# Kernel optimization log

Hardware: AMD Instinct MI355X
Metric: run time of the kernel (lower is better)

The kernel has to match this reference:

```python
import jax, jax.numpy as jnp
import numpy as np

N_NODES = 50000


def _glorot(key, fan_in, fan_out):
    lim = jnp.sqrt(6.0 / (fan_in + fan_out)).astype(jnp.float32)
    return jax.random.uniform(key, (fan_in, fan_out), jnp.float32, -lim, lim)


def gcn_layer(x, W, b, src, dst, deg_inv_sqrt):
    # PyG GCNConv: x' = D^{-1/2} (A + I) D^{-1/2} (x W) + b
    h = x @ W  # [N, F_out]
    norm = deg_inv_sqrt[src] * deg_inv_sqrt[dst]  # [E+N]
    msg = norm[:, None] * h[src]                  # gather + scale
    out = jax.ops.segment_sum(msg, dst, num_segments=x.shape[0])
    return out + b


def setup_inputs() -> dict:
    key = jax.random.key(0)
    ks = jax.random.split(key, 8)
    in_c, out_c = 128, 64
    hid = 2 * out_c
    x = jax.random.normal(ks[0], (N_NODES, in_c), jnp.float32)
    edge_index = jax.random.randint(ks[1], (2, 800000), 0, N_NODES, jnp.int64)
    return {
        "x": x,
        "edge_index": edge_index,
        "W1": _glorot(ks[2], in_c, hid), "b1": jnp.zeros((hid,), jnp.float32),
        "W2": _glorot(ks[3], hid, hid),  "b2": jnp.zeros((hid,), jnp.float32),
        "W3": _glorot(ks[4], hid, out_c), "b3": jnp.zeros((out_c,), jnp.float32),
    }


def reference(x, edge_index, W1, b1, W2, b2, W3, b3):
    n = x.shape[0]
    loops = jnp.arange(n, dtype=edge_index.dtype)
    src = jnp.concatenate([edge_index[0], loops])  # [E+N]
    dst = jnp.concatenate([edge_index[1], loops])
    deg = jax.ops.segment_sum(jnp.ones_like(dst, dtype=x.dtype), dst, num_segments=n)
    deg_inv_sqrt = jnp.where(deg > 0, jax.lax.rsqrt(deg), 0.0)

    h = jax.nn.relu(gcn_layer(x, W1, b1, src, dst, deg_inv_sqrt))
    h = jax.nn.relu(gcn_layer(h, W2, b2, src, dst, deg_inv_sqrt))
    return gcn_layer(h, W3, b3, src, dst, deg_inv_sqrt)
```

## Files before the change

kernel.cpp:

```cpp
#include <hip/hip_runtime.h>
#include <hip/hip_bf16.h>
#include <hip/hip_fp16.h>
#include <cstdint>
#include <cstddef>

typedef _Float16 half8_t __attribute__((ext_vector_type(8)));
typedef float f32x4 __attribute__((ext_vector_type(4)));
typedef unsigned short ushort8_v __attribute__((ext_vector_type(8)));


__global__ __launch_bounds__(256) void prep_kernel(int* __restrict__ cnt, int N4,
                                                   const float* __restrict__ W1, _Float16* __restrict__ wt1,
                                                   const float* __restrict__ W2, _Float16* __restrict__ wt2,
                                                   const float* __restrict__ W3, _Float16* __restrict__ wt3,
                                                   _Float16* __restrict__ gA, _Float16* __restrict__ gB,
                                                   _Float16* __restrict__ gC, int N) {
  int i = blockIdx.x * 256 + threadIdx.x;
  if (i < N4) {
    *(int4*)&cnt[i * 4] = make_int4(0, 0, 0, 0);
    return;
  }
  int j = i - N4;
  if (j < 16384) {
    int k = j >> 7, c = j & 127;
    wt1[c * 128 + k] = (_Float16)W1[j];
    return;
  }
  j -= 16384;
  if (j < 16384) {
    int k = j >> 7, c = j & 127;
    wt2[c * 128 + k] = (_Float16)W2[j];
    return;
  }
  j -= 16384;
  if (j < 8192) {
    int k = j >> 6, c = j & 63;
    wt3[c * 128 + k] = (_Float16)W3[j];
    return;
  }
  j -= 8192;
  if (j < 40) {
    half8_t z = {};
    if (j < 16)       *(half8_t*)&gA[(size_t)N * 128 + j * 8] = z;
    else if (j < 32)  *(half8_t*)&gB[(size_t)N * 128 + (j - 16) * 8] = z;
    else              *(half8_t*)&gC[(size_t)N * 64 + (j - 32) * 8] = z;
  }
}


__global__ __launch_bounds__(256) void countpos_fill_kernel(const int* __restrict__ dst,
                                                            int* __restrict__ cnt,
                                                            ushort* __restrict__ pos, int E,
                                                            int* __restrict__ ssInt, int ssInts,
                                                            int countBlocks, int fillPat) {
  if (blockIdx.x >= countBlocks) {
    int f = ((blockIdx.x - countBlocks) * 256 + threadIdx.x) * 4;
    if (f + 4 <= ssInts) *(int4*)&ssInt[f] = make_int4(fillPat, fillPat, fillPat, fillPat);
    else for (; f < ssInts; ++f) ssInt[f] = fillPat;
    return;
  }
  int e = (blockIdx.x * blockDim.x + threadIdx.x) * 2;
  if (e + 2 <= E) {
    int2 d = *(const int2*)&dst[e];
    int p0 = atomicAdd(&cnt[d.x], 1);
    int p1 = atomicAdd(&cnt[d.y], 1);
    ushort2 pk;
    pk.x = (ushort)p0; pk.y = (ushort)p1;
    *(ushort2*)&pos[e] = pk;
  } else {
    for (; e < E; ++e) pos[e] = (ushort)atomicAdd(&cnt[dst[e]], 1);
  }
}


__global__ __launch_bounds__(256) void block_sum_kernel(const int* __restrict__ cnt,
                                                        int* __restrict__ bsum, int N) {
  const int tid = threadIdx.x, lane = tid & 63, wid = tid >> 6;
  __shared__ int wt[4];
  int base = blockIdx.x * 2048 + tid * 8;
  int s = 0;
#pragma unroll
  for (int q = 0; q < 8; ++q) { int i = base + q; if (i < N) s += (cnt[i] + 7) & ~7; }
#pragma unroll
  for (int off = 32; off; off >>= 1) s += __shfl_down(s, off);
  if (lane == 0) wt[wid] = s;
  __syncthreads();
  if (tid == 0) bsum[blockIdx.x] = wt[0] + wt[1] + wt[2] + wt[3];
}

__global__ __launch_bounds__(256) void scan_bsum_kernel(const int* __restrict__ bsum,
                                                        int* __restrict__ boff,
                                                        int NB, int* __restrict__ rpN) {
  __shared__ int sh[256];
  const int tid = threadIdx.x;
  int v = (tid < NB) ? bsum[tid] : 0;
  sh[tid] = v;
  __syncthreads();
  for (int off = 1; off < 256; off <<= 1) {
    int t = (tid >= off) ? sh[tid - off] : 0;
    __syncthreads();
    sh[tid] += t;
    __syncthreads();
  }
  if (tid < NB) boff[tid] = sh[tid] - v;
  if (tid == 255) rpN[0] = sh[255];
}

__global__ __launch_bounds__(256) void scan_apply_kernel(const int* __restrict__ cnt,
                                                         const int* __restrict__ boff,
                                                         int* __restrict__ rp,
                                                         float* __restrict__ dis, int N) {
  const int tid = threadIdx.x, lane = tid & 63, wid = tid >> 6;
  __shared__ int wtot[4], wexc[4];
  int base = blockIdx.x * 2048 + tid * 8;
  int v[8]; int s = 0;
#pragma unroll
  for (int q = 0; q < 8; ++q) {
    int i = base + q; int x = (i < N) ? cnt[i] : 0;
    v[q] = x; s += (x + 7) & ~7;
  }
  int sc = s;
#pragma unroll
  for (int off = 1; off < 64; off <<= 1) { int t = __shfl_up(sc, off); if (lane >= off) sc += t; }
  if (lane == 63) wtot[wid] = sc;
  __syncthreads();
  if (tid == 0) { int r = 0; for (int wq = 0; wq < 4; ++wq) { wexc[wq] = r; r += wtot[wq]; } }
  __syncthreads();
  int thr = boff[blockIdx.x] + wexc[wid] + (sc - s);
#pragma unroll
  for (int q = 0; q < 8; ++q) {
    int i = base + q;
    if (i < N) { rp[i] = thr; dis[i] = rsqrtf((float)(v[q] + 1)); }
    thr += (v[q] + 7) & ~7;
  }
}


__global__ __launch_bounds__(256) void place_gemm1_kernel(const int* __restrict__ src,
                                                          const int* __restrict__ dst,
                                                          const ushort* __restrict__ pos,
                                                          const int* __restrict__ rp,
                                                          ushort* __restrict__ ss, int E,
                                                          const float* __restrict__ X,
                                                          const half8_t* __restrict__ Wt,
                                                          const float* __restrict__ dis,
                                                          _Float16* __restrict__ G, int N,
                                                          int gemmBlocks) {
  if (blockIdx.x >= gemmBlocks) {
    int e = ((blockIdx.x - gemmBlocks) * blockDim.x + threadIdx.x) * 4;
    if (e + 4 <= E) {
      int4 d = *(const int4*)&dst[e];
      ushort4 p = *(const ushort4*)&pos[e];
      int4 s = *(const int4*)&src[e];
      int r0 = rp[d.x], r1 = rp[d.y], r2 = rp[d.z], r3 = rp[d.w];
      ss[r0 + p.x] = (ushort)s.x;
      ss[r1 + p.y] = (ushort)s.y;
      ss[r2 + p.z] = (ushort)s.z;
      ss[r3 + p.w] = (ushort)s.w;
    } else {
      for (; e < E; ++e) ss[rp[dst[e]] + pos[e]] = (ushort)src[e];
    }
    return;
  }
  const int wave = threadIdx.x >> 6;
  const int lane = threadIdx.x & 63;
  const int wm = wave >> 1, wn = wave & 1;
  const int row0 = blockIdx.x * 128 + wm * 64;
  const int col0 = wn * 64;
  const int lr = lane & 15;
  const int lk = lane >> 4;
  f32x4 acc[4][4];
#pragma unroll
  for (int r = 0; r < 4; ++r)
#pragma unroll
    for (int c = 0; c < 4; ++c) acc[r][c] = (f32x4){0.f, 0.f, 0.f, 0.f};

#pragma unroll
  for (int ks = 0; ks < 4; ++ks) {
    half8_t a[4], b[4];
#pragma unroll
    for (int r = 0; r < 4; ++r) {
      int row = row0 + r * 16 + lr;
      half8_t av = {};
      if (row < N) {
        const float* xp = &X[(size_t)row * 128 + ks * 32 + lk * 8];
        float4 xa = *(const float4*)xp;
        float4 xb = *(const float4*)(xp + 4);
        av[0] = (_Float16)xa.x; av[1] = (_Float16)xa.y; av[2] = (_Float16)xa.z; av[3] = (_Float16)xa.w;
        av[4] = (_Float16)xb.x; av[5] = (_Float16)xb.y; av[6] = (_Float16)xb.z; av[7] = (_Float16)xb.w;
      }
      a[r] = av;
    }
#pragma unroll
    for (int c = 0; c < 4; ++c) {
      int col = col0 + c * 16 + lr;
      b[c] = Wt[(size_t)col * 16 + ks * 4 + lk];
    }
#pragma unroll
    for (int r = 0; r < 4; ++r)
#pragma unroll
      for (int c = 0; c < 4; ++c)
        acc[r][c] = __builtin_amdgcn_mfma_f32_16x16x32_f16(a[r], b[c], acc[r][c], 0, 0, 0);
  }

#pragma unroll
  for (int r = 0; r < 4; ++r) {
#pragma unroll
    for (int q = 0; q < 4; ++q) {
      int row = row0 + r * 16 + lk * 4 + q;
      if (row < N) {
        float dv = dis[row];
#pragma unroll
        for (int c = 0; c < 4; ++c)
          G[(size_t)row * 128 + col0 + c * 16 + lr] = (_Float16)(acc[r][c][q] * dv);
      }
    }
  }
}


template <int COUT>
__global__ __launch_bounds__(256) void fused_agg_gemm_kernel(const _Float16* __restrict__ G,
                                                             const int* __restrict__ rp,
                                                             const ushort* __restrict__ ss,
                                                             const float* __restrict__ dis,
                                                             const float* __restrict__ bias,
                                                             const half8_t* __restrict__ Wt,
                                                             _Float16* __restrict__ G2, int N) {
  __shared__ _Float16 sh[32][136];
  const int wave = threadIdx.x >> 6;
  const int lane = threadIdx.x & 63;
  const int grp = lane >> 4;
  const int sub = lane & 15;
  const int nb0 = blockIdx.x * 32;

#pragma unroll
  for (int it = 0; it < 2; ++it) {
    const int wl = it * 16 + wave * 4 + grp;
    const int w = nb0 + wl;
    if (w < N) {
      const int e0 = rp[w], e1 = rp[w + 1];
      float acc[8];
      half8_t sv = *(const half8_t*)&G[(size_t)w * 128 + sub * 8];
#pragma unroll
      for (int j = 0; j < 8; ++j) acc[j] = (float)sv[j];
      for (int e = e0; e < e1; e += 8) {
        ushort8_v iv = *(const ushort8_v*)&ss[e];
        half8_t v[8];
#pragma unroll
        for (int q = 0; q < 8; ++q) v[q] = *(const half8_t*)&G[(size_t)iv[q] * 128 + sub * 8];
#pragma unroll
        for (int j = 0; j < 8; ++j)
          acc[j] += (((float)v[0][j] + (float)v[1][j]) + ((float)v[2][j] + (float)v[3][j])) +
                    (((float)v[4][j] + (float)v[5][j]) + ((float)v[6][j] + (float)v[7][j]));
      }
      float d = dis[w];
      float4 b0 = *(const float4*)&bias[sub * 8];
      float4 b1 = *(const float4*)&bias[sub * 8 + 4];
      float bb[8] = {b0.x, b0.y, b0.z, b0.w, b1.x, b1.y, b1.z, b1.w};
      half8_t o;
#pragma unroll
      for (int j = 0; j < 8; ++j) {
        float v = fmaxf(d * acc[j] + bb[j], 0.f);
        o[j] = (_Float16)v;
      }
      *(half8_t*)&sh[wl][sub * 8] = o;
    }
  }
  __syncthreads();

  const int lr = lane & 15;
  const int lk = lane >> 4;
  constexpr int NC = COUT / 64;
  const int col0 = wave * (COUT / 4);
  f32x4 acc2[2][NC];
#pragma unroll
  for (int r = 0; r < 2; ++r)
#pragma unroll
    for (int c = 0; c < NC; ++c) acc2[r][c] = (f32x4){0.f, 0.f, 0.f, 0.f};

#pragma unroll
  for (int ks = 0; ks < 4; ++ks) {
    half8_t a[2], b[NC];
#pragma unroll
    for (int r = 0; r < 2; ++r)
      a[r] = *(const half8_t*)&sh[r * 16 + lr][ks * 32 + lk * 8];
#pragma unroll
    for (int c = 0; c < NC; ++c) {
      int col = col0 + c * 16 + lr;
      b[c] = Wt[(size_t)col * 16 + ks * 4 + lk];
    }
#pragma unroll
    for (int r = 0; r < 2; ++r)
#pragma unroll
      for (int c = 0; c < NC; ++c)
        acc2[r][c] = __builtin_amdgcn_mfma_f32_16x16x32_f16(a[r], b[c], acc2[r][c], 0, 0, 0);
  }

#pragma unroll
  for (int r = 0; r < 2; ++r) {
#pragma unroll
    for (int q = 0; q < 4; ++q) {
      int row = nb0 + r * 16 + lk * 4 + q;
      if (row < N) {
        float dv = dis[row];
#pragma unroll
        for (int c = 0; c < NC; ++c)
          G2[(size_t)row * COUT + col0 + c * 16 + lr] = (_Float16)(acc2[r][c][q] * dv);
      }
    }
  }
}


__global__ __launch_bounds__(256) void agg64_kernel(const _Float16* __restrict__ G,
                                                    const int* __restrict__ rp,
                                                    const ushort* __restrict__ ss,
                                                    const float* __restrict__ dis,
                                                    const float* __restrict__ bias,
                                                    float* __restrict__ OUT, int N) {
  const int wave = threadIdx.x >> 6;
  const int lane = threadIdx.x & 63;
  const int grp = lane >> 3;
  const int sub = lane & 7;
  const int w = blockIdx.x * 32 + wave * 8 + grp;
  if (w >= N) return;
  const int e0 = rp[w], e1 = rp[w + 1];
  float acc[8];
  half8_t sv = *(const half8_t*)&G[(size_t)w * 64 + sub * 8];
#pragma unroll
  for (int j = 0; j < 8; ++j) acc[j] = (float)sv[j];
  for (int e = e0; e < e1; e += 8) {
    ushort8_v iv = *(const ushort8_v*)&ss[e];
    half8_t v[8];
#pragma unroll
    for (int q = 0; q < 8; ++q) v[q] = *(const half8_t*)&G[(size_t)iv[q] * 64 + sub * 8];
#pragma unroll
    for (int j = 0; j < 8; ++j)
      acc[j] += (((float)v[0][j] + (float)v[1][j]) + ((float)v[2][j] + (float)v[3][j])) +
                (((float)v[4][j] + (float)v[5][j]) + ((float)v[6][j] + (float)v[7][j]));
  }
  float d = dis[w];
  float4 b0 = *(const float4*)&bias[sub * 8];
  float4 b1 = *(const float4*)&bias[sub * 8 + 4];
  float4 o0, o1;
  o0.x = d * acc[0] + b0.x; o0.y = d * acc[1] + b0.y;
  o0.z = d * acc[2] + b0.z; o0.w = d * acc[3] + b0.w;
  o1.x = d * acc[4] + b1.x; o1.y = d * acc[5] + b1.y;
  o1.z = d * acc[6] + b1.z; o1.w = d * acc[7] + b1.w;
  *(float4*)&OUT[(size_t)w * 64 + sub * 8] = o0;
  *(float4*)&OUT[(size_t)w * 64 + sub * 8 + 4] = o1;
}


extern "C" void kernel_launch(void* const* d_in, const int* in_sizes, int n_in,
                              void* d_out, int out_size, void* d_ws, size_t ws_size,
                              hipStream_t stream) {
  const float* x  = (const float*)d_in[0];
  const int*   ei = (const int*)d_in[1];
  const float* W1 = (const float*)d_in[2];
  const float* b1 = (const float*)d_in[3];
  const float* W2 = (const float*)d_in[4];
  const float* b2 = (const float*)d_in[5];
  const float* W3 = (const float*)d_in[6];
  const float* b3 = (const float*)d_in[7];

  const int inC = in_sizes[2] / in_sizes[3];
  const int N = in_sizes[0] / inC;
  const int E = in_sizes[1] / 2;

  const int SSPAD = ((E + 7 * N + 8) + 7) & ~7;

  auto align256 = [](size_t v) { return (v + 255) & ~(size_t)255; };
  char* p = (char*)d_ws;
  int* cnt = (int*)p;   p += align256((size_t)N * 4);
  int* rp  = (int*)p;   p += align256((size_t)(N + 1) * 4);
  ushort* ss = (ushort*)p;  p += align256((size_t)SSPAD * 2);
  ushort* pos = (ushort*)p; p += align256((size_t)E * 2);
  float* dis = (float*)p; p += align256((size_t)N * 4);
  _Float16* gA = (_Float16*)p; p += align256((size_t)(N + 1) * 128 * 2);
  _Float16* gB = (_Float16*)p; p += align256((size_t)(N + 1) * 128 * 2);
  _Float16* gC = (_Float16*)p; p += align256((size_t)(N + 1) * 64 * 2);
  _Float16* wt1 = (_Float16*)p; p += align256((size_t)128 * 128 * 2);
  _Float16* wt2 = (_Float16*)p; p += align256((size_t)128 * 128 * 2);
  _Float16* wt3 = (_Float16*)p; p += align256((size_t)64 * 128 * 2);
  int* bsum = (int*)p;  p += align256(1024 * 4);
  int* boff = (int*)p;  p += align256(1024 * 4);

  const int* srcv = ei;
  const int* dstv = ei + E;

  const int NB = (N + 2047) / 2048;
  const int eB2 = (E / 2 + 255) / 256;
  const int eB4 = (E / 4 + 255) / 256;
  const int N4 = (N + 3) / 4;
  const int prepTot = N4 + 16384 + 16384 + 8192 + 40;
  const int ssInts = SSPAD / 2;
  const int fillB = (ssInts / 4 + 255) / 256;
  const int fillPat = (int)(((unsigned)N) | (((unsigned)N) << 16));

  prep_kernel<<<(prepTot + 255) / 256, 256, 0, stream>>>(cnt, N4, W1, wt1, W2, wt2, W3, wt3,
                                                         gA, gB, gC, N);
  countpos_fill_kernel<<<eB2 + fillB, 256, 0, stream>>>(dstv, cnt, pos, E,
                                                        (int*)ss, ssInts, eB2, fillPat);
  block_sum_kernel<<<NB, 256, 0, stream>>>(cnt, bsum, N);
  scan_bsum_kernel<<<1, 256, 0, stream>>>(bsum, boff, NB, rp + N);
  scan_apply_kernel<<<NB, 256, 0, stream>>>(cnt, boff, rp, dis, N);

  const int g1B = (N + 127) / 128;
  const int fB  = (N + 31) / 32;
  const int a64B = (N + 31) / 32;

  place_gemm1_kernel<<<g1B + eB4, 256, 0, stream>>>(srcv, dstv, pos, rp, ss, E,
                                                    x, (const half8_t*)wt1, dis, gA, N, g1B);
  fused_agg_gemm_kernel<128><<<fB, 256, 0, stream>>>(gA, rp, ss, dis, b1, (const half8_t*)wt2, gB, N);
  fused_agg_gemm_kernel<64><<<fB, 256, 0, stream>>>(gB, rp, ss, dis, b2, (const half8_t*)wt3, gC, N);
  agg64_kernel<<<a64B, 256, 0, stream>>>(gC, rp, ss, dis, b3, (float*)d_out, N);
}
```

Measured before the change: 167.9 us.

## Split feature columns into passes and spread edges across lanes in aggregation

Both aggregation kernels now go over the feature dimension in 32-column passes (four for the 128-wide layer, two for the 64-wide output). Within each pass, lanes that used to cover distinct feature slices are split into edge-parallel groups, with partial sums combined through xor shuffles. The intent is to keep each pass's gather working set small so neighbor rows stay in cache, and to cut per-lane outstanding loads and register pressure. In exchange, the index array and row offsets are re-read on every pass, shuffle reductions are added, and only a quarter or half of the lanes do the epilogue.

```diff
diff --git a/kernel.cpp b/kernel.cpp
--- a/kernel.cpp
+++ b/kernel.cpp
@@ -232,39 +232,53 @@
   const int lane = threadIdx.x & 63;
   const int grp = lane >> 4;
   const int sub = lane & 15;
+  const int ep = sub >> 2;
+  const int fq = sub & 3;
   const int nb0 = blockIdx.x * 32;
 
 #pragma unroll
-  for (int it = 0; it < 2; ++it) {
-    const int wl = it * 16 + wave * 4 + grp;
-    const int w = nb0 + wl;
-    if (w < N) {
-      const int e0 = rp[w], e1 = rp[w + 1];
-      float acc[8];
-      half8_t sv = *(const half8_t*)&G[(size_t)w * 128 + sub * 8];
-#pragma unroll
-      for (int j = 0; j < 8; ++j) acc[j] = (float)sv[j];
-      for (int e = e0; e < e1; e += 8) {
-        ushort8_v iv = *(const ushort8_v*)&ss[e];
-        half8_t v[8];
-#pragma unroll
-        for (int q = 0; q < 8; ++q) v[q] = *(const half8_t*)&G[(size_t)iv[q] * 128 + sub * 8];
-#pragma unroll
-        for (int j = 0; j < 8; ++j)
-          acc[j] += (((float)v[0][j] + (float)v[1][j]) + ((float)v[2][j] + (float)v[3][j])) +
-                    (((float)v[4][j] + (float)v[5][j]) + ((float)v[6][j] + (float)v[7][j]));
+  for (int pass = 0; pass < 4; ++pass) {
+#pragma unroll
+    for (int it = 0; it < 2; ++it) {
+      const int wl = it * 16 + wave * 4 + grp;
+      const int w = nb0 + wl;
+      if (w < N) {
+        const int e0 = rp[w], e1 = rp[w + 1];
+        float acc[8];
+        if (ep == 0) {
+          half8_t sv = *(const half8_t*)&G[(size_t)w * 128 + pass * 32 + fq * 8];
+#pragma unroll
+          for (int j = 0; j < 8; ++j) acc[j] = (float)sv[j];
+        } else {
+#pragma unroll
+          for (int j = 0; j < 8; ++j) acc[j] = 0.f;
+        }
+        for (int e = e0; e < e1; e += 8) {
+          ushort8_v iv = *(const ushort8_v*)&ss[e];
+          int j0 = iv[ep], j1 = iv[4 + ep];
+          half8_t v0 = *(const half8_t*)&G[(size_t)j0 * 128 + pass * 32 + fq * 8];
+          half8_t v1 = *(const half8_t*)&G[(size_t)j1 * 128 + pass * 32 + fq * 8];
+#pragma unroll
+          for (int j = 0; j < 8; ++j) acc[j] += (float)v0[j] + (float)v1[j];
+        }
+#pragma unroll
+        for (int j = 0; j < 8; ++j) acc[j] += __shfl_xor(acc[j], 4);
+#pragma unroll
+        for (int j = 0; j < 8; ++j) acc[j] += __shfl_xor(acc[j], 8);
+        if (ep == 0) {
+          float d = dis[w];
+          float4 b0 = *(const float4*)&bias[pass * 32 + fq * 8];
+          float4 b1 = *(const float4*)&bias[pass * 32 + fq * 8 + 4];
+          float bb[8] = {b0.x, b0.y, b0.z, b0.w, b1.x, b1.y, b1.z, b1.w};
+          half8_t o;
+#pragma unroll
+          for (int j = 0; j < 8; ++j) {
+            float v = fmaxf(d * acc[j] + bb[j], 0.f);
+            o[j] = (_Float16)v;
+          }
+          *(half8_t*)&sh[wl][pass * 32 + fq * 8] = o;
+        }
       }
-      float d = dis[w];
-      float4 b0 = *(const float4*)&bias[sub * 8];
-      float4 b1 = *(const float4*)&bias[sub * 8 + 4];
-      float bb[8] = {b0.x, b0.y, b0.z, b0.w, b1.x, b1.y, b1.z, b1.w};
-      half8_t o;
-#pragma unroll
-      for (int j = 0; j < 8; ++j) {
-        float v = fmaxf(d * acc[j] + bb[j], 0.f);
-        o[j] = (_Float16)v;
-      }
-      *(half8_t*)&sh[wl][sub * 8] = o;
     }
   }
   __syncthreads();
@@ -323,33 +337,48 @@
   const int lane = threadIdx.x & 63;
   const int grp = lane >> 3;
   const int sub = lane & 7;
+  const int ep2 = sub >> 2;
+  const int fq = sub & 3;
   const int w = blockIdx.x * 32 + wave * 8 + grp;
   if (w >= N) return;
   const int e0 = rp[w], e1 = rp[w + 1];
-  float acc[8];
-  half8_t sv = *(const half8_t*)&G[(size_t)w * 64 + sub * 8];
-#pragma unroll
-  for (int j = 0; j < 8; ++j) acc[j] = (float)sv[j];
-  for (int e = e0; e < e1; e += 8) {
-    ushort8_v iv = *(const ushort8_v*)&ss[e];
-    half8_t v[8];
-#pragma unroll
-    for (int q = 0; q < 8; ++q) v[q] = *(const half8_t*)&G[(size_t)iv[q] * 64 + sub * 8];
-#pragma unroll
-    for (int j = 0; j < 8; ++j)
-      acc[j] += (((float)v[0][j] + (float)v[1][j]) + ((float)v[2][j] + (float)v[3][j])) +
-                (((float)v[4][j] + (float)v[5][j]) + ((float)v[6][j] + (float)v[7][j]));
-  }
-  float d = dis[w];
-  float4 b0 = *(const float4*)&bias[sub * 8];
-  float4 b1 = *(const float4*)&bias[sub * 8 + 4];
-  float4 o0, o1;
-  o0.x = d * acc[0] + b0.x; o0.y = d * acc[1] + b0.y;
-  o0.z = d * acc[2] + b0.z; o0.w = d * acc[3] + b0.w;
-  o1.x = d * acc[4] + b1.x; o1.y = d * acc[5] + b1.y;
-  o1.z = d * acc[6] + b1.z; o1.w = d * acc[7] + b1.w;
-  *(float4*)&OUT[(size_t)w * 64 + sub * 8] = o0;
-  *(float4*)&OUT[(size_t)w * 64 + sub * 8 + 4] = o1;
+  const float d = dis[w];
+
+#pragma unroll
+  for (int pass = 0; pass < 2; ++pass) {
+    float acc[8];
+    if (ep2 == 0) {
+      half8_t sv = *(const half8_t*)&G[(size_t)w * 64 + pass * 32 + fq * 8];
+#pragma unroll
+      for (int j = 0; j < 8; ++j) acc[j] = (float)sv[j];
+    } else {
+#pragma unroll
+      for (int j = 0; j < 8; ++j) acc[j] = 0.f;
+    }
+    for (int e = e0; e < e1; e += 8) {
+      ushort8_v iv = *(const ushort8_v*)&ss[e];
+#pragma unroll
+      for (int q = 0; q < 4; ++q) {
+        int jj = iv[q * 2 + ep2];
+        half8_t v = *(const half8_t*)&G[(size_t)jj * 64 + pass * 32 + fq * 8];
+#pragma unroll
+        for (int j = 0; j < 8; ++j) acc[j] += (float)v[j];
+      }
+    }
+#pragma unroll
+    for (int j = 0; j < 8; ++j) acc[j] += __shfl_xor(acc[j], 4);
+    if (ep2 == 0) {
+      float4 b0 = *(const float4*)&bias[pass * 32 + fq * 8];
+      float4 b1 = *(const float4*)&bias[pass * 32 + fq * 8 + 4];
+      float4 o0, o1;
+      o0.x = d * acc[0] + b0.x; o0.y = d * acc[1] + b0.y;
+      o0.z = d * acc[2] + b0.z; o0.w = d * acc[3] + b0.w;
+      o1.x = d * acc[4] + b1.x; o1.y = d * acc[5] + b1.y;
+      o1.z = d * acc[6] + b1.z; o1.w = d * acc[7] + b1.w;
+      *(float4*)&OUT[(size_t)w * 64 + pass * 32 + fq * 8] = o0;
+      *(float4*)&OUT[(size_t)w * 64 + pass * 32 + fq * 8 + 4] = o1;
+    }
+  }
 }
 
 
```

Result: slower. 190.9 us (+13.7%).
